# Kernel tuning notes

Hardware: AMD Instinct MI355X
Metric: run time of the kernel (lower is better)

Reference implementation:

```python
import jax, jax.numpy as jnp
import numpy as np

B, C, H, W = 4, 64, 64, 64
E = 64            # embed_dim
K_TOP = 128       # k (init arg), K_TOP <= N
N = H * W


def conv2d(x, w, b, pad):
    # x: [B,C,H,W], w: [O,I,kh,kw]
    y = jax.lax.conv_general_dilated(
        x, w, window_strides=(1, 1), padding=[(pad, pad), (pad, pad)],
        dimension_numbers=('NCHW', 'OIHW', 'NCHW'))
    return y + b[None, :, None, None]


def setup_inputs() -> dict:
    key = jax.random.key(0)
    ks = jax.random.split(key, 16)
    def w_init(k, shape, fan_in):
        return jax.random.normal(k, shape, jnp.float32) * (1.0 / np.sqrt(fan_in))
    return {
        'x':  jax.random.normal(ks[0], (B, C, H, W), jnp.float32),
        'w1': w_init(ks[1], (C, C, 1, 1), C),
        'b1': jnp.zeros((C,), jnp.float32),
        'w3': w_init(ks[2], (C, C, 3, 3), C * 9),
        'b3': jnp.zeros((C,), jnp.float32),
        'w5': w_init(ks[3], (C, C, 5, 5), C * 25),
        'b5': jnp.zeros((C,), jnp.float32),
        'wq': w_init(ks[4], (3 * C, E), 3 * C),
        'bq': jnp.zeros((E,), jnp.float32),
        'wk': w_init(ks[5], (3 * C, E), 3 * C),
        'bk': jnp.zeros((E,), jnp.float32),
        'wv': w_init(ks[6], (3 * C, C), 3 * C),
        'bv': jnp.zeros((C,), jnp.float32),
        'wo': w_init(ks[7], (C, C), C),
        'bo': jnp.zeros((C,), jnp.float32),
    }


def reference(x, w1, b1, w3, b3, w5, b5, wq, bq, wk, bk, wv, bv, wo, bo):
    b, c, h, w = x.shape
    n = h * w
    # multi-scale conv paths
    f1 = conv2d(x, w1, b1, 0)
    f2 = conv2d(x, w3, b3, 1)
    f3 = conv2d(x, w5, b5, 2)
    f_multi = jnp.concatenate([f1, f2, f3], axis=1)          # [B,3C,H,W]
    f_flat = f_multi.reshape(b, 3 * c, n).transpose(0, 2, 1)  # [B,N,3C]
    Q = f_flat @ wq + bq                                      # [B,N,E]
    Kt = f_flat @ wk + bk                                     # [B,N,E]
    V = f_flat @ wv + bv                                      # [B,N,C]
    attn = jnp.einsum('bqe,bke->bqk', Q, Kt) / np.sqrt(E)     # [B,N,N]
    attn = jax.nn.softmax(attn, axis=-1)
    key_importance = attn.sum(axis=1)                         # [B,N]
    _, topk_idx = jax.lax.top_k(key_importance, K_TOP)        # [B,K]
    mask = jnp.zeros_like(key_importance)
    mask = mask.at[jnp.arange(b)[:, None], topk_idx].set(1.0)  # [B,N]
    out = jnp.einsum('bqk,bkc->bqc', attn * mask[:, None, :], V)  # [B,N,C]
    out = out @ wo + bo
    return out.transpose(0, 2, 1).reshape(b, c, h, w)
```

## Files before the change

### kernel.cpp

```cpp
#include <hip/hip_runtime.h>
#include <math.h>

#define N_PIX 4096
#define CCH 64

typedef __attribute__((ext_vector_type(8))) short short8;
typedef __attribute__((ext_vector_type(4))) float f32x4;
typedef __attribute__((ext_vector_type(16))) float f32x16;

#define EXP2C 0.18033688f

__device__ __forceinline__ int swz(int row, int col) {
  return row * 68 + (col ^ (((row >> 2) & 7) << 2));
}

__device__ __forceinline__ float fget(const float4& v, int j) {
  return ((const float*)&v)[j];
}

__device__ __forceinline__ unsigned short f2bf(float f) {
  unsigned u = __float_as_uint(f);
  unsigned r = (u + 0x7fff + ((u >> 16) & 1)) >> 16;
  return (unsigned short)r;
}
__device__ __forceinline__ float bf2f(unsigned short h) {
  return __uint_as_float((unsigned)h << 16);
}

__device__ __forceinline__ void gll16(const unsigned short* g, unsigned short* lbase,
                                      int lane) {
#if __has_builtin(__builtin_amdgcn_global_load_lds)
  (void)lane;
  __builtin_amdgcn_global_load_lds(
      (const __attribute__((address_space(1))) void*)g,
      (__attribute__((address_space(3))) void*)lbase, 16, 0, 0);
#else
  *(short8*)(lbase + lane * 8) = *(const short8*)g;
#endif
}

__global__ __launch_bounds__(256) void prep_kernel(
    const float* __restrict__ w1, const float* __restrict__ w3,
    const float* __restrict__ w5, const float* __restrict__ wq,
    const float* __restrict__ wk, const float* __restrict__ wv,
    unsigned short* __restrict__ Bfh, unsigned short* __restrict__ Bfl) {
  __shared__ float At[64 * 68];
  __shared__ float Bt[64 * 68];
  const int which = blockIdx.x, t = blockIdx.y;
  const int ky = t / 5, kx = t % 5;
  const float* Wsel = which == 0 ? wq : (which == 1 ? wk : wv);
  const bool in3 = (ky >= 1 && ky <= 3 && kx >= 1 && kx <= 3);
  const bool c1 = (t == 12);
  const int t3 = (ky - 1) * 3 + (kx - 1);
  const int tid = threadIdx.x, tx = tid & 15, ty = tid >> 4;
  float acc[4][4];
#pragma unroll
  for (int i = 0; i < 4; ++i)
#pragma unroll
    for (int j = 0; j < 4; ++j) acc[i][j] = 0.f;
  const int npass = 1 + (in3 ? 1 : 0) + (c1 ? 1 : 0);
  for (int pass = 0; pass < npass; ++pass) {
    const int kind = pass == 0 ? 0 : (pass == 1 && in3 ? 1 : 2);
    const int rowbase = kind == 0 ? 128 : (kind == 1 ? 64 : 0);
    __syncthreads();
    for (int v = tid; v < 4096; v += 256) {
      const int i = v & 63, o = v >> 6;
      float a;
      if (kind == 0) a = w5[(size_t)(o * 64 + i) * 25 + t];
      else if (kind == 1) a = w3[(size_t)(o * 64 + i) * 9 + t3];
      else a = w1[o * 64 + i];
      At[swz(i, o)] = a;
    }
    for (int v = tid; v < 1024; v += 256) {
      const int row = v >> 4, c4 = (v & 15) * 4;
      *(float4*)&Bt[swz(row, c4)] = *(const float4*)(Wsel + (rowbase + row) * 64 + c4);
    }
    __syncthreads();
#pragma unroll
    for (int o4 = 0; o4 < 16; ++o4) {
      float4 a[4], b[4];
#pragma unroll
      for (int i = 0; i < 4; ++i) a[i] = *(const float4*)&At[swz(ty * 4 + i, o4 * 4)];
#pragma unroll
      for (int u = 0; u < 4; ++u) b[u] = *(const float4*)&Bt[swz(o4 * 4 + u, tx * 4)];
#pragma unroll
      for (int i = 0; i < 4; ++i)
#pragma unroll
        for (int j = 0; j < 4; ++j)
#pragma unroll
          for (int u = 0; u < 4; ++u)
            acc[i][j] = fmaf(fget(a[i], u), fget(b[u], j), acc[i][j]);
    }
  }
#pragma unroll
  for (int ii = 0; ii < 4; ++ii) {
    const int i = ty * 4 + ii;
    const int s = i >> 5, lg = (i >> 3) & 3, j = i & 7;
#pragma unroll
    for (int jj = 0; jj < 4; ++jj) {
      const int em = tx * 4 + jj;
      const int q = which * 4 + (em >> 4), lr = em & 15;
      const size_t off = ((size_t)(t * 12 + q) * 2 + s) * 512 + (lg * 16 + lr) * 8 + j;
      const float val = acc[ii][jj];
      const unsigned short h = f2bf(val);
      Bfh[off] = h;
      Bfl[off] = f2bf(val - bf2f(h));
    }
  }
}

__global__ __launch_bounds__(192) void beff_kernel(
    const float* __restrict__ b1, const float* __restrict__ b3,
    const float* __restrict__ b5, const float* __restrict__ bq,
    const float* __restrict__ bk, const float* __restrict__ bv,
    const float* __restrict__ wq, const float* __restrict__ wk,
    const float* __restrict__ wv, float* __restrict__ beff) {
  const int e = threadIdx.x;
  const int em = e & 63, which = e >> 6;
  const float* Wsel = which == 0 ? wq : (which == 1 ? wk : wv);
  const float* bsel = which == 0 ? bq : (which == 1 ? bk : bv);
  float s = bsel[em];
  for (int row = 0; row < 192; ++row) {
    const float bc = row < 64 ? b1[row] : (row < 128 ? b3[row - 64] : b5[row - 128]);
    s += bc * Wsel[row * 64 + em];
  }
  beff[e] = s;
}

__global__ __launch_bounds__(256) void xpose_kernel(const float* __restrict__ x,
                                                    unsigned short* __restrict__ Xth,
                                                    unsigned short* __restrict__ Xtl) {
  __shared__ float t[64][65];
  const int yp = blockIdx.x;
  const int b = blockIdx.y;
  const int tid = threadIdx.x;
  const size_t rowbase = ((size_t)b * 68 + yp) * 72 * 64;
  short8 z8 = {0, 0, 0, 0, 0, 0, 0, 0};
  if (yp < 2 || yp >= 66) {
    short8* ph = (short8*)(Xth + rowbase);
    short8* pl = (short8*)(Xtl + rowbase);
    for (int v = tid; v < 576; v += 256) {
      ph[v] = z8;
      pl[v] = z8;
    }
    return;
  }
  const int y = yp - 2;
  for (int it = 0; it < 16; ++it) {
    const int v = it * 256 + tid;
    const int c = v >> 6, xx = v & 63;
    t[xx][c] = x[(((size_t)b * 64 + c) * 64 + y) * 64 + xx];
  }
  for (int s = tid; s < 64; s += 256) {
    const int col = s >> 3;
    const int xp = col < 2 ? col : col + 64;
    const size_t o = rowbase + (size_t)xp * 64 + (s & 7) * 8;
    *(short8*)(Xth + o) = z8;
    *(short8*)(Xtl + o) = z8;
  }
  __syncthreads();
  for (int it = 0; it < 16; ++it) {
    const int v = it * 256 + tid;
    const int xx = v >> 6, c = v & 63;
    const float val = t[xx][c];
    const unsigned short h = f2bf(val);
    const unsigned short lo = f2bf(val - bf2f(h));
    const int xp = xx + 2;
    const size_t idx = rowbase + (size_t)xp * 64 + (c ^ ((xp & 7) << 3));
    Xth[idx] = h;
    Xtl[idx] = lo;
  }
}

__global__ __launch_bounds__(256) void fused_qkv_kernel(
    const unsigned short* __restrict__ Xth, const unsigned short* __restrict__ Xtl,
    const unsigned short* __restrict__ Bfh, const unsigned short* __restrict__ Bfl,
    const float* __restrict__ beff, unsigned short* __restrict__ Qhi,
    unsigned short* __restrict__ Qlo, unsigned short* __restrict__ Khi,
    unsigned short* __restrict__ Klo, float* __restrict__ Vm) {
  __shared__ unsigned short Lh[192 * 64];
  __shared__ unsigned short Ll[192 * 64];
  const int b = blockIdx.y, sb = blockIdx.x;
  const int y0 = (sb >> 3) * 8, x0 = (sb & 7) * 8;
  const int tid = threadIdx.x, wv = tid >> 6, l = tid & 63;
  const int lr = l & 15, lg = l >> 4;
  const int qd = blockIdx.z * 4 + wv;
#pragma unroll
  for (int rr = 0; rr < 3; ++rr) {
    const int py = wv * 3 + rr;
    const size_t src = (((size_t)b * 68 + y0 + py) * 72 + x0) * 64 + (size_t)l * 8;
    gll16(Xth + src, &Lh[py * 1024], l);
    gll16(Xth + src + 512, &Lh[py * 1024 + 512], l);
    gll16(Xtl + src, &Ll[py * 1024], l);
    gll16(Xtl + src + 512, &Ll[py * 1024 + 512], l);
  }
  __syncthreads();
  f32x4 acc[4];
#pragma unroll
  for (int pg = 0; pg < 4; ++pg) acc[pg] = (f32x4){0.f, 0.f, 0.f, 0.f};
  for (int ky = 0; ky < 5; ++ky) {
    for (int kx = 0; kx < 5; ++kx) {
      const int t = ky * 5 + kx;
      const size_t f = ((size_t)(t * 12 + qd)) * 2;
      const short8 bh0 = *(const short8*)&Bfh[f * 512 + l * 8];
      const short8 bh1 = *(const short8*)&Bfh[(f + 1) * 512 + l * 8];
      const short8 bl0 = *(const short8*)&Bfl[f * 512 + l * 8];
      const short8 bl1 = *(const short8*)&Bfl[(f + 1) * 512 + l * 8];
#pragma unroll
      for (int pg = 0; pg < 4; ++pg) {
        const int p = pg * 16 + lr;
        const int prt = ((p >> 3) + ky) * 16 + (p & 7) + kx;
        const int rb = prt * 64, sw = (prt & 7) << 3;
        const short8 ah0 = *(const short8*)&Lh[rb + ((lg * 8) ^ sw)];
        const short8 ah1 = *(const short8*)&Lh[rb + ((32 + lg * 8) ^ sw)];
        const short8 al0 = *(const short8*)&Ll[rb + ((lg * 8) ^ sw)];
        const short8 al1 = *(const short8*)&Ll[rb + ((32 + lg * 8) ^ sw)];
        acc[pg] = __builtin_amdgcn_mfma_f32_16x16x32_bf16(ah0, bh0, acc[pg], 0, 0, 0);
        acc[pg] = __builtin_amdgcn_mfma_f32_16x16x32_bf16(ah1, bh1, acc[pg], 0, 0, 0);
        acc[pg] = __builtin_amdgcn_mfma_f32_16x16x32_bf16(al0, bh0, acc[pg], 0, 0, 0);
        acc[pg] = __builtin_amdgcn_mfma_f32_16x16x32_bf16(al1, bh1, acc[pg], 0, 0, 0);
        acc[pg] = __builtin_amdgcn_mfma_f32_16x16x32_bf16(ah0, bl0, acc[pg], 0, 0, 0);
        acc[pg] = __builtin_amdgcn_mfma_f32_16x16x32_bf16(ah1, bl1, acc[pg], 0, 0, 0);
      }
    }
  }
  const size_t base = (size_t)b * N_PIX;
  {
    const int e = qd * 16 + lr;
    const int which = e >> 6, em = e & 63;
    const float be = beff[e];
#pragma unroll
    for (int pg = 0; pg < 4; ++pg) {
#pragma unroll
      for (int r = 0; r < 4; ++r) {
        const int pp = pg * 16 + lg * 4 + r;
        const int n = (y0 + (pp >> 3)) * 64 + x0 + (pp & 7);
        const float val = acc[pg][r] + be;
        const size_t off = (base + n) * 64 + em;
        if (which == 2) {
          Vm[off] = val;
        } else {
          const unsigned short h = f2bf(val);
          const unsigned short lo = f2bf(val - bf2f(h));
          if (which == 0) {
            Qhi[off] = h;
            Qlo[off] = lo;
          } else {
            Khi[off] = h;
            Klo[off] = lo;
          }
        }
      }
    }
  }
}

__global__ __launch_bounds__(256) void qk_s_kernel(
    const unsigned short* __restrict__ Qhi, const unsigned short* __restrict__ Qlo,
    const unsigned short* __restrict__ Khi, const unsigned short* __restrict__ Klo,
    float* __restrict__ s_part) {
  __shared__ unsigned short Kst[2][2][2048];
  const int b = blockIdx.z, kc = blockIdx.y, q0 = blockIdx.x * 128;
  const int tid = threadIdx.x, wv = tid >> 6, l = tid & 63;
  const int lr = l & 31, lh = l >> 5;
  const size_t base = (size_t)b * N_PIX;
  const size_t qoff = (base + q0 + wv * 32 + lr) * 64 + lh * 8;
  short8 qh[4], ql[4];
#pragma unroll
  for (int f = 0; f < 4; ++f) {
    qh[f] = *(const short8*)(Qhi + qoff + f * 16);
    ql[f] = *(const short8*)(Qlo + qoff + f * 16);
  }
  const int srow = tid >> 3;
  const int gcu = ((tid & 7) * 8) ^ ((srow & 7) << 3);
  const unsigned short* Ksh = Khi + (base + kc * 512 + srow) * 64 + gcu;
  const unsigned short* Ksl = Klo + (base + kc * 512 + srow) * 64 + gcu;
  float racc[16];
#pragma unroll
  for (int r = 0; r < 16; ++r) racc[r] = 0.f;

#define STAGE(bb, t)                                   \
  {                                                    \
    const size_t go_ = (size_t)(t) * 2048;             \
    gll16(Ksh + go_, &Kst[bb][0][wv * 512], l);        \
    gll16(Ksl + go_, &Kst[bb][1][wv * 512], l);        \
  }
#define COMP(bb)                                                                     \
  {                                                                                  \
    short8 kh_[4], kl_[4];                                                           \
    const int rb_ = lr * 64, sw_ = (lr & 7) << 3;                                    \
    _Pragma("unroll") for (int f = 0; f < 4; ++f) {                                  \
      const int c_ = rb_ + ((lh * 8 + f * 16) ^ sw_);                                \
      kh_[f] = *(const short8*)&Kst[bb][0][c_];                                      \
      kl_[f] = *(const short8*)&Kst[bb][1][c_];                                      \
    }                                                                                \
    f32x16 acc;                                                                      \
    _Pragma("unroll") for (int r = 0; r < 16; ++r) acc[r] = 0.f;                     \
    _Pragma("unroll") for (int f = 0; f < 4; ++f)                                    \
        acc = __builtin_amdgcn_mfma_f32_32x32x16_bf16(qh[f], kh_[f], acc, 0, 0, 0);  \
    _Pragma("unroll") for (int f = 0; f < 4; ++f)                                    \
        acc = __builtin_amdgcn_mfma_f32_32x32x16_bf16(ql[f], kh_[f], acc, 0, 0, 0);  \
    _Pragma("unroll") for (int f = 0; f < 4; ++f)                                    \
        acc = __builtin_amdgcn_mfma_f32_32x32x16_bf16(qh[f], kl_[f], acc, 0, 0, 0);  \
    _Pragma("unroll") for (int r = 0; r < 16; ++r)                                   \
        racc[r] += exp2f(acc[r] * EXP2C);                                            \
  }

  STAGE(0, 0);
  __syncthreads();
  int bu = 0;
  for (int t = 0; t < 16; ++t) {
    if (t < 15) STAGE(bu ^ 1, t + 1);
    COMP(bu);
    __syncthreads();
    bu ^= 1;
  }
#undef STAGE
#undef COMP
#pragma unroll
  for (int r = 0; r < 16; ++r)
#pragma unroll
    for (int m = 1; m < 32; m <<= 1) racc[r] += __shfl_xor(racc[r], m);
  if (lr == 0) {
#pragma unroll
    for (int r = 0; r < 16; ++r) {
      const int row = (r & 3) + 8 * (r >> 2) + 4 * lh;
      s_part[((size_t)(b * 8 + kc) << 12) + q0 + wv * 32 + row] = racc[r];
    }
  }
}

__global__ __launch_bounds__(256) void combine_kernel(const float* __restrict__ s_part,
                                                      float* __restrict__ invs,
                                                      float* __restrict__ lg2w) {
  const int g = blockIdx.x * 256 + threadIdx.x;
  const int b = g >> 12, q = g & 4095;
  float s = 0.f;
#pragma unroll
  for (int kc = 0; kc < 8; ++kc) s += s_part[((size_t)(b * 8 + kc) << 12) + q];
  invs[g] = 1.f / s;
  lg2w[g] = -__log2f(s);
}

__global__ __launch_bounds__(256) void colsum_kernel2(
    const unsigned short* __restrict__ Qhi, const unsigned short* __restrict__ Qlo,
    const unsigned short* __restrict__ Khi, const unsigned short* __restrict__ Klo,
    const float* __restrict__ lg2w, float* __restrict__ cs_part) {
  __shared__ unsigned short Qst[2][2][2048];
  const int b = blockIdx.z, qc = blockIdx.y, k0 = blockIdx.x * 128;
  const int tid = threadIdx.x, wv = tid >> 6, l = tid & 63;
  const int lr = l & 31, lh = l >> 5;
  const size_t base = (size_t)b * N_PIX;
  const size_t koff = (base + k0 + wv * 32 + lr) * 64 + lh * 8;
  short8 kh[4], kl[4];
#pragma unroll
  for (int f = 0; f < 4; ++f) {
    kh[f] = *(const short8*)(Khi + koff + f * 16);
    kl[f] = *(const short8*)(Klo + koff + f * 16);
  }
  const int srow = tid >> 3;
  const int gcu = ((tid & 7) * 8) ^ ((srow & 7) << 3);
  const unsigned short* Qsh = Qhi + (base + qc * 512 + srow) * 64 + gcu;
  const unsigned short* Qsl = Qlo + (base + qc * 512 + srow) * 64 + gcu;
  const float* lwp = lg2w + b * N_PIX + qc * 512 + lr;
  float kacc[16];
#pragma unroll
  for (int r = 0; r < 16; ++r) kacc[r] = 0.f;

#define STAGE(bb, t)                                   \
  {                                                    \
    const size_t go_ = (size_t)(t) * 2048;             \
    gll16(Qsh + go_, &Qst[bb][0][wv * 512], l);        \
    gll16(Qsl + go_, &Qst[bb][1][wv * 512], l);        \
  }
#define COMP(bb, lw_)                                                                \
  {                                                                                  \
    short8 qh_[4], ql_[4];                                                           \
    const int rb_ = lr * 64, sw_ = (lr & 7) << 3;                                    \
    _Pragma("unroll") for (int f = 0; f < 4; ++f) {                                  \
      const int c_ = rb_ + ((lh * 8 + f * 16) ^ sw_);                                \
      qh_[f] = *(const short8*)&Qst[bb][0][c_];                                      \
      ql_[f] = *(const short8*)&Qst[bb][1][c_];                                      \
    }                                                                                \
    f32x16 acc;                                                                      \
    _Pragma("unroll") for (int r = 0; r < 16; ++r) acc[r] = 0.f;                     \
    _Pragma("unroll") for (int f = 0; f < 4; ++f)                                    \
        acc = __builtin_amdgcn_mfma_f32_32x32x16_bf16(kh[f], qh_[f], acc, 0, 0, 0);  \
    _Pragma("unroll") for (int f = 0; f < 4; ++f)                                    \
        acc = __builtin_amdgcn_mfma_f32_32x32x16_bf16(kl[f], qh_[f], acc, 0, 0, 0);  \
    _Pragma("unroll") for (int f = 0; f < 4; ++f)                                    \
        acc = __builtin_amdgcn_mfma_f32_32x32x16_bf16(kh[f], ql_[f], acc, 0, 0, 0);  \
    _Pragma("unroll") for (int r = 0; r < 16; ++r)                                   \
        kacc[r] += exp2f(fmaf(acc[r], EXP2C, lw_));                                  \
  }

  STAGE(0, 0);
  float lwa = lwp[0], lwb;
  __syncthreads();
  int bu = 0;
  for (int t = 0; t < 16; ++t) {
    if (t < 15) {
      STAGE(bu ^ 1, t + 1);
      lwb = lwp[(t + 1) * 32];
    }
    COMP(bu, lwa);
    lwa = lwb;
    __syncthreads();
    bu ^= 1;
  }
#undef STAGE
#undef COMP
#pragma unroll
  for (int r = 0; r < 16; ++r)
#pragma unroll
    for (int m = 1; m < 32; m <<= 1) kacc[r] += __shfl_xor(kacc[r], m);
  if (lr == 0) {
#pragma unroll
    for (int r = 0; r < 16; ++r) {
      const int row = (r & 3) + 8 * (r >> 2) + 4 * lh;
      cs_part[((size_t)(b * 8 + qc) << 12) + k0 + wv * 32 + row] = kacc[r];
    }
  }
}

__global__ __launch_bounds__(256) void topk_kernel(const float* __restrict__ cs_part,
                                                   int* __restrict__ topk) {
  __shared__ unsigned keys[4096];
  __shared__ unsigned hist[256];
  __shared__ unsigned sbuf[256];
  __shared__ unsigned selB, selNeed;
  const int b = blockIdx.x, tid = threadIdx.x;
  for (int v = tid; v < 4096; v += 256) {
    float s = 0.f;
#pragma unroll
    for (int qc = 0; qc < 8; ++qc) s += cs_part[((size_t)(b * 8 + qc) << 12) + v];
    unsigned u = __float_as_uint(s);
    keys[v] = (u & 0x80000000u) ? ~u : (u | 0x80000000u);
  }
  unsigned need = 128, prefix = 0;
  __syncthreads();
  for (int d = 3; d >= 0; --d) {
    const int shift = d * 8;
    hist[tid] = 0;
    __syncthreads();
    for (int v = tid; v < 4096; v += 256) {
      const unsigned k = keys[v];
      if (d == 3 || (k >> (shift + 8)) == prefix)
        atomicAdd(&hist[(k >> shift) & 255], 1u);
    }
    __syncthreads();
    sbuf[tid] = hist[tid];
    __syncthreads();
    for (int off = 1; off < 256; off <<= 1) {
      const unsigned add = (tid + off < 256) ? sbuf[tid + off] : 0;
      __syncthreads();
      sbuf[tid] += add;
      __syncthreads();
    }
    const unsigned sufGe = sbuf[tid];
    const unsigned sufGt = (tid < 255) ? sbuf[tid + 1] : 0;
    if (sufGt < need && need <= sufGe) {
      selB = (unsigned)tid;
      selNeed = need - sufGt;
    }
    __syncthreads();
    prefix = (prefix << 8) | selB;
    need = selNeed;
    __syncthreads();
  }
  const unsigned T = prefix;
  unsigned gtc = 0, eqc = 0;
#pragma unroll
  for (int j = 0; j < 16; ++j) {
    const unsigned k = keys[tid * 16 + j];
    gtc += (k > T);
    eqc += (k == T);
  }
  sbuf[tid] = (gtc << 16) | eqc;
  __syncthreads();
  for (int off = 1; off < 256; off <<= 1) {
    const unsigned add = (tid >= off) ? sbuf[tid - off] : 0;
    __syncthreads();
    sbuf[tid] += add;
    __syncthreads();
  }
  const unsigned incl = sbuf[tid];
  const unsigned gBase = (incl >> 16) - gtc;
  const unsigned eBase = (incl & 0xffffu) - eqc;
  const unsigned nGt = sbuf[255] >> 16;
  unsigned g = 0, e = 0;
#pragma unroll
  for (int j = 0; j < 16; ++j) {
    const int idx = tid * 16 + j;
    const unsigned k = keys[idx];
    if (k > T) {
      topk[b * 128 + gBase + g] = idx;
      ++g;
    } else if (k == T) {
      if (eBase + e < need) topk[b * 128 + nGt + eBase + e] = idx;
      ++e;
    }
  }
}

__global__ __launch_bounds__(256) void attn_out_kernel(
    const unsigned short* __restrict__ Qhp, const unsigned short* __restrict__ Qlp,
    const unsigned short* __restrict__ Khp, const unsigned short* __restrict__ Klp,
    const float* __restrict__ Vm, const float* __restrict__ invs,
    const int* __restrict__ topkb, const float* __restrict__ wo,
    const float* __restrict__ bo, float* __restrict__ dout) {
  __shared__ float Qld[32 * 68], Kld[64 * 68], Vt[64 * 68], Pl[32 * 68], Wl[64 * 68];
  __shared__ int sidx[64];
  const int b = blockIdx.y, q0 = blockIdx.x * 32;
  const int tid = threadIdx.x, tx = tid & 15, ty = tid >> 4;
  const size_t base = (size_t)b * N_PIX;
  for (int v = tid; v < 512; v += 256) {
    int row = v >> 4, c4 = (v & 15) * 4;
    size_t off = (base + q0 + row) * 64 + c4;
    ushort4 h = *(const ushort4*)(Qhp + off);
    ushort4 lo = *(const ushort4*)(Qlp + off);
    float4 f;
    f.x = bf2f(h.x) + bf2f(lo.x);
    f.y = bf2f(h.y) + bf2f(lo.y);
    f.z = bf2f(h.z) + bf2f(lo.z);
    f.w = bf2f(h.w) + bf2f(lo.w);
    *(float4*)&Qld[swz(row, c4)] = f;
  }
  for (int v = tid; v < 1024; v += 256) {
    int row = v >> 4, c4 = (v & 15) * 4;
    *(float4*)&Wl[swz(row, c4)] = *(const float4*)(wo + row * 64 + c4);
  }
  float is[2];
#pragma unroll
  for (int i = 0; i < 2; ++i) is[i] = invs[base + q0 + ty * 2 + i];
  float acc[2][4];
#pragma unroll
  for (int i = 0; i < 2; ++i)
#pragma unroll
    for (int j = 0; j < 4; ++j) acc[i][j] = 0.f;
  for (int ch = 0; ch < 2; ++ch) {
    __syncthreads();
    if (tid < 64) sidx[tid] = topkb[b * 128 + ch * 64 + tid];
    __syncthreads();
    for (int v = tid; v < 1024; v += 256) {
      int row = v >> 4, c4 = (v & 15) * 4;
      size_t off = (base + sidx[row]) * 64 + c4;
      ushort4 h = *(const ushort4*)(Khp + off);
      ushort4 lo = *(const ushort4*)(Klp + off);
      float4 f;
      f.x = bf2f(h.x) + bf2f(lo.x);
      f.y = bf2f(h.y) + bf2f(lo.y);
      f.z = bf2f(h.z) + bf2f(lo.z);
      f.w = bf2f(h.w) + bf2f(lo.w);
      *(float4*)&Kld[swz(row, c4)] = f;
    }
    for (int v = tid; v < 4096; v += 256) {
      int row = v >> 6, c = v & 63;
      Vt[swz(c, row)] = Vm[(base + sidx[row]) * 64 + c];
    }
    __syncthreads();
    float z[2][4];
#pragma unroll
    for (int i = 0; i < 2; ++i)
#pragma unroll
      for (int j = 0; j < 4; ++j) z[i][j] = 0.f;
#pragma unroll
    for (int e4 = 0; e4 < 16; ++e4) {
      float4 qa[2], ka[4];
#pragma unroll
      for (int i = 0; i < 2; ++i) qa[i] = *(const float4*)&Qld[swz(ty * 2 + i, e4 * 4)];
#pragma unroll
      for (int j = 0; j < 4; ++j) ka[j] = *(const float4*)&Kld[swz(tx * 4 + j, e4 * 4)];
#pragma unroll
      for (int i = 0; i < 2; ++i)
#pragma unroll
        for (int j = 0; j < 4; ++j)
#pragma unroll
          for (int u = 0; u < 4; ++u)
            z[i][j] = fmaf(fget(qa[i], u), fget(ka[j], u), z[i][j]);
    }
#pragma unroll
    for (int i = 0; i < 2; ++i)
#pragma unroll
      for (int j = 0; j < 4; ++j)
        Pl[swz(ty * 2 + i, tx * 4 + j)] = __expf(z[i][j] * 0.125f) * is[i];
    __syncthreads();
#pragma unroll
    for (int k4 = 0; k4 < 16; ++k4) {
      float4 pr[2], vr[4];
#pragma unroll
      for (int i = 0; i < 2; ++i) pr[i] = *(const float4*)&Pl[swz(ty * 2 + i, k4 * 4)];
#pragma unroll
      for (int j = 0; j < 4; ++j) vr[j] = *(const float4*)&Vt[swz(tx * 4 + j, k4 * 4)];
#pragma unroll
      for (int i = 0; i < 2; ++i)
#pragma unroll
        for (int j = 0; j < 4; ++j)
#pragma unroll
          for (int u = 0; u < 4; ++u)
            acc[i][j] = fmaf(fget(pr[i], u), fget(vr[j], u), acc[i][j]);
    }
  }
  __syncthreads();
#pragma unroll
  for (int i = 0; i < 2; ++i)
#pragma unroll
    for (int j = 0; j < 4; ++j) Pl[swz(ty * 2 + i, tx * 4 + j)] = acc[i][j];
  __syncthreads();
  float yacc[2][4];
#pragma unroll
  for (int i = 0; i < 2; ++i)
#pragma unroll
    for (int j = 0; j < 4; ++j) yacc[i][j] = 0.f;
#pragma unroll
  for (int e4 = 0; e4 < 16; ++e4) {
    float4 a[2], wr[4];
#pragma unroll
    for (int i = 0; i < 2; ++i) a[i] = *(const float4*)&Pl[swz(ty * 2 + i, e4 * 4)];
#pragma unroll
    for (int u = 0; u < 4; ++u) wr[u] = *(const float4*)&Wl[swz(e4 * 4 + u, tx * 4)];
#pragma unroll
    for (int i = 0; i < 2; ++i)
#pragma unroll
      for (int j = 0; j < 4; ++j)
#pragma unroll
        for (int u = 0; u < 4; ++u)
          yacc[i][j] = fmaf(fget(a[i], u), fget(wr[u], j), yacc[i][j]);
  }
  __syncthreads();
#pragma unroll
  for (int i = 0; i < 2; ++i)
#pragma unroll
    for (int j = 0; j < 4; ++j)
      Qld[swz(ty * 2 + i, tx * 4 + j)] = yacc[i][j] + bo[tx * 4 + j];
  __syncthreads();
  for (int v = tid; v < 2048; v += 256) {
    int c = v >> 5, nl = v & 31;
    dout[((size_t)b * 64 + c) * 4096 + q0 + nl] = Qld[swz(nl, c)];
  }
}

extern "C" void kernel_launch(void* const* d_in, const int* in_sizes, int n_in,
                              void* d_out, int out_size, void* d_ws, size_t ws_size,
                              hipStream_t stream) {
  const float* x = (const float*)d_in[0];
  const float* w1 = (const float*)d_in[1];
  const float* b1 = (const float*)d_in[2];
  const float* w3 = (const float*)d_in[3];
  const float* b3 = (const float*)d_in[4];
  const float* w5 = (const float*)d_in[5];
  const float* b5 = (const float*)d_in[6];
  const float* wq = (const float*)d_in[7];
  const float* bq = (const float*)d_in[8];
  const float* wk = (const float*)d_in[9];
  const float* bk = (const float*)d_in[10];
  const float* wv = (const float*)d_in[11];
  const float* bv = (const float*)d_in[12];
  const float* wo = (const float*)d_in[13];
  const float* bo = (const float*)d_in[14];

  const size_t BN = (size_t)4 * N_PIX;
  char* p = (char*)d_ws;
  auto carve = [&](size_t bytes) -> void* {
    void* r = (void*)p;
    p += (bytes + 255) & ~(size_t)255;
    return r;
  };
  unsigned short* Bfh = (unsigned short*)carve((size_t)25 * 12 * 2 * 512 * 2);
  unsigned short* Bfl = (unsigned short*)carve((size_t)25 * 12 * 2 * 512 * 2);
  float* beff = (float*)carve(192 * 4);
  unsigned short* Xth = (unsigned short*)carve((size_t)4 * 68 * 72 * 64 * 2);
  unsigned short* Xtl = (unsigned short*)carve((size_t)4 * 68 * 72 * 64 * 2);
  float* Vm = (float*)carve(BN * 64 * 4);
  unsigned short* Qhi = (unsigned short*)carve(BN * 64 * 2);
  unsigned short* Qlo = (unsigned short*)carve(BN * 64 * 2);
  unsigned short* Khi = (unsigned short*)carve(BN * 64 * 2);
  unsigned short* Klo = (unsigned short*)carve(BN * 64 * 2);
  float* s_part = (float*)carve((size_t)4 * 8 * 4096 * 4);
  float* invs = (float*)carve(BN * 4);
  float* lg2w = (float*)carve(BN * 4);
  float* cs_part = (float*)carve((size_t)4 * 8 * 4096 * 4);
  int* topkbuf = (int*)carve(512 * 4);

  prep_kernel<<<dim3(3, 25), 256, 0, stream>>>(w1, w3, w5, wq, wk, wv, Bfh, Bfl);
  beff_kernel<<<1, 192, 0, stream>>>(b1, b3, b5, bq, bk, bv, wq, wk, wv, beff);
  xpose_kernel<<<dim3(68, 4), 256, 0, stream>>>(x, Xth, Xtl);
  fused_qkv_kernel<<<dim3(64, 4, 3), 256, 0, stream>>>(Xth, Xtl, Bfh, Bfl, beff, Qhi,
                                                       Qlo, Khi, Klo, Vm);
  qk_s_kernel<<<dim3(32, 8, 4), 256, 0, stream>>>(Qhi, Qlo, Khi, Klo, s_part);
  combine_kernel<<<64, 256, 0, stream>>>(s_part, invs, lg2w);
  colsum_kernel2<<<dim3(32, 8, 4), 256, 0, stream>>>(Qhi, Qlo, Khi, Klo, lg2w, cs_part);
  topk_kernel<<<4, 256, 0, stream>>>(cs_part, topkbuf);
  attn_out_kernel<<<dim3(128, 4), 256, 0, stream>>>(Qhi, Qlo, Khi, Klo, Vm, invs,
                                                    topkbuf, wo, bo, (float*)d_out);
}
```

Before: 182.5 us.

## Deepen LDS staging to four buffers and process two tiles per barrier

The QK row-sum kernel and the column-sum kernel now use four LDS buffers instead of two. Each iteration stages two tiles ahead and computes two tiles, so the number of __syncthreads drops by half and loads get more time to land before they are used. The loop is fully unrolled, and the per-tile log-weight load moves inside COMP. LDS use per block doubles to 32KB, which may lower occupancy, and unrolling raises register pressure.

```diff
diff --git a/kernel.cpp b/kernel.cpp
--- a/kernel.cpp
+++ b/kernel.cpp
@@ -259,7 +259,7 @@
     const unsigned short* __restrict__ Qhi, const unsigned short* __restrict__ Qlo,
     const unsigned short* __restrict__ Khi, const unsigned short* __restrict__ Klo,
     float* __restrict__ s_part) {
-  __shared__ unsigned short Kst[2][2][2048];
+  __shared__ unsigned short Kst[4][2][2048];
   const int b = blockIdx.z, kc = blockIdx.y, q0 = blockIdx.x * 128;
   const int tid = threadIdx.x, wv = tid >> 6, l = tid & 63;
   const int lr = l & 31, lh = l >> 5;
@@ -307,13 +307,15 @@
   }
 
   STAGE(0, 0);
-  __syncthreads();
-  int bu = 0;
-  for (int t = 0; t < 16; ++t) {
-    if (t < 15) STAGE(bu ^ 1, t + 1);
-    COMP(bu);
-    __syncthreads();
-    bu ^= 1;
+  STAGE(1, 1);
+  __syncthreads();
+#pragma unroll
+  for (int t = 0; t < 16; t += 2) {
+    if (t + 2 < 16) STAGE((t + 2) & 3, t + 2);
+    if (t + 3 < 16) STAGE((t + 3) & 3, t + 3);
+    COMP(t & 3);
+    COMP((t + 1) & 3);
+    __syncthreads();
   }
 #undef STAGE
 #undef COMP
@@ -346,7 +348,7 @@
     const unsigned short* __restrict__ Qhi, const unsigned short* __restrict__ Qlo,
     const unsigned short* __restrict__ Khi, const unsigned short* __restrict__ Klo,
     const float* __restrict__ lg2w, float* __restrict__ cs_part) {
-  __shared__ unsigned short Qst[2][2][2048];
+  __shared__ unsigned short Qst[4][2][2048];
   const int b = blockIdx.z, qc = blockIdx.y, k0 = blockIdx.x * 128;
   const int tid = threadIdx.x, wv = tid >> 6, l = tid & 63;
   const int lr = l & 31, lh = l >> 5;
@@ -373,8 +375,9 @@
     gll16(Qsh + go_, &Qst[bb][0][wv * 512], l);        \
     gll16(Qsl + go_, &Qst[bb][1][wv * 512], l);        \
   }
-#define COMP(bb, lw_)                                                                \
+#define COMP(bb, t_)                                                                 \
   {                                                                                  \
+    const float lw_ = lwp[(t_) * 32];                                                \
     short8 qh_[4], ql_[4];                                                           \
     const int rb_ = lr * 64, sw_ = (lr & 7) << 3;                                    \
     _Pragma("unroll") for (int f = 0; f < 4; ++f) {                                  \
@@ -395,18 +398,15 @@
   }
 
   STAGE(0, 0);
-  float lwa = lwp[0], lwb;
-  __syncthreads();
-  int bu = 0;
-  for (int t = 0; t < 16; ++t) {
-    if (t < 15) {
-      STAGE(bu ^ 1, t + 1);
-      lwb = lwp[(t + 1) * 32];
-    }
-    COMP(bu, lwa);
-    lwa = lwb;
-    __syncthreads();
-    bu ^= 1;
+  STAGE(1, 1);
+  __syncthreads();
+#pragma unroll
+  for (int t = 0; t < 16; t += 2) {
+    if (t + 2 < 16) STAGE((t + 2) & 3, t + 2);
+    if (t + 3 < 16) STAGE((t + 3) & 3, t + 3);
+    COMP(t & 3, t);
+    COMP((t + 1) & 3, t + 1);
+    __syncthreads();
   }
 #undef STAGE
 #undef COMP
```

Result: slower. 187.4 us (+2.7%).
